# Optimization experiments

Measured on AMD Instinct MI355X. Metric: run time of the kernel, lower is better.

## Reference

```python
import jax, jax.numpy as jnp
import numpy as np

# Dimensions: B batches, E links, T time steps, F flows, rank-r factors, K unrolled iters
B, E, T, F = 16, 256, 4096, 512
RANK = 10
NUM_ITER = 5


def setup_inputs() -> dict:
    key = jax.random.key(0)
    ks = jax.random.split(key, 9)
    Y = jax.random.normal(ks[0], (B, E, T), dtype=jnp.float32)
    R = (jax.random.uniform(ks[1], (B, E, F)) < 0.1).astype(jnp.float32)
    Omega = (jax.random.uniform(ks[2], (B, E, T)) < 0.9).astype(jnp.float32)
    P0 = jax.random.normal(ks[3], (B, E, RANK), dtype=jnp.float32) * 0.1
    Q0 = jax.random.normal(ks[4], (B, T, RANK), dtype=jnp.float32) * 0.1
    # per-iteration learned log-parameters of the unrolled network
    lam_log = jax.random.normal(ks[5], (NUM_ITER,), dtype=jnp.float32) * 0.1 - 1.0
    mu_log = jax.random.normal(ks[6], (NUM_ITER,), dtype=jnp.float32) * 0.1 - 1.0
    nu_log = jax.random.normal(ks[7], (NUM_ITER,), dtype=jnp.float32) * 0.1
    gamma_logit = jax.random.normal(ks[8], (NUM_ITER,), dtype=jnp.float32) * 0.1
    return {"Y": Y, "R": R, "Omega": Omega, "P0": P0, "Q0": Q0,
            "lam_log": lam_log, "mu_log": mu_log, "nu_log": nu_log,
            "gamma_logit": gamma_logit}


def reference(Y, R, Omega, P0, Q0, lam_log, mu_log, nu_log, gamma_logit):
    """Unrolled BSCA: Y ~ X + R @ A + noise on observed entries (Omega mask),
    X relaxed low-rank via factors P (B,E,r), Q (B,T,r); A sparse anomalies (B,F,T).
    Each iteration: rank-r ridge solves for P and Q (left=False -> rhs @ inv(lhs)),
    relaxed X update, soft-thresholded BSCA direction for A + convex-combination step."""
    rank = P0.shape[-1]
    eye = jnp.eye(rank, dtype=Y.dtype)
    X = Omega * Y                     # (B,E,T) init relaxed variable
    A = jnp.zeros((*Y.shape[:-2], R.shape[-1], Y.shape[-1]), dtype=Y.dtype)  # (B,F,T)
    P, Q = P0, Q0
    A_scale = (R * R).mT @ (Omega * Omega)          # (B,F,T)
    noobs = A_scale == 0
    A_scale_safe = A_scale + noobs.astype(Y.dtype)
    for k in range(NUM_ITER):
        lam = jnp.exp(lam_log[k])
        mu = jnp.exp(mu_log[k])
        nu = jnp.exp(nu_log[k])
        gamma = jax.nn.sigmoid(gamma_logit[k])
        regp = lam / nu
        # P update: P = (X @ Q) @ inv(Q^T Q + regp I)   (right solve; lhs symmetric)
        lhsQ = Q.mT @ Q + regp * eye                 # (B,r,r)
        P = jnp.linalg.solve(lhsQ, (X @ Q).mT).mT    # (B,E,r)
        # Q update: Q = (X^T @ P) @ inv(P^T P + regp I)
        lhsP = P.mT @ P + regp * eye
        Q = jnp.linalg.solve(lhsP, (X.mT @ P).mT).mT # (B,T,r)
        # X update (relaxed): X = (Omega*err + nu*P Q^T) / (Omega^2 + nu)
        RA = R @ A                                   # (B,E,T)
        err = Omega * (Y - RA)
        X = (Omega * err + nu * (P @ Q.mT)) / (Omega * Omega + nu)
        # A update: soft-thresholded best-response + convex combination step
        resid = Omega * (Y - X - RA)                 # (B,E,T)
        BA = A + (R.mT @ resid) / A_scale_safe       # (B,F,T)
        A_dir = jnp.sign(BA) * jnp.maximum(jnp.abs(BA) - mu / A_scale_safe, 0.0)
        A_dir = jnp.where(noobs, 0.0, A_dir)
        A = A + gamma * (A_dir - A)
    return A
```

## Files before the change

### kernel.cpp

```cpp
#include <hip/hip_runtime.h>
#include <stdint.h>

#define BB 16
#define EE 256
#define TT 4096
#define FF 512
#define RK 10
#define NIT 5

typedef short bf16x8 __attribute__((ext_vector_type(8)));
typedef float f32x4  __attribute__((ext_vector_type(4)));

__device__ __forceinline__ unsigned short f2bf(float x){
  unsigned int u = __float_as_uint(x);
  unsigned int r = (u + 0x7FFFu + ((u >> 16) & 1u)) >> 16;
  return (unsigned short)r;
}
__device__ __forceinline__ float bf2f(unsigned short s){
  return __uint_as_float(((unsigned int)s) << 16);
}

__device__ __forceinline__ void gld16(const void* g, void* l){
  __builtin_amdgcn_global_load_lds((const __attribute__((address_space(1))) unsigned int*)g,
                                   (__attribute__((address_space(3))) unsigned int*)l,
                                   16, 0, 0);
}


__global__ void k_params(const float* lam_log, const float* mu_log,
                         const float* nu_log, const float* gl, float* prm){
  int k = threadIdx.x;
  if (k < NIT){
    float lam = expf(lam_log[k]);
    float mu  = expf(mu_log[k]);
    float nu  = expf(nu_log[k]);
    float gam = 1.0f/(1.0f+expf(-gl[k]));
    prm[k*8+0]=lam; prm[k*8+1]=mu; prm[k*8+2]=nu; prm[k*8+3]=gam; prm[k*8+4]=lam/nu;
  }
}

__global__ void k_initX(const float4* __restrict__ Y, const float4* __restrict__ Om,
                        float4* __restrict__ X, ushort4* __restrict__ Omb){
  int i = blockIdx.x*256 + threadIdx.x;
  float4 y = Y[i], o = Om[i];
  X[i] = make_float4(y.x*o.x, y.y*o.y, y.z*o.z, y.w*o.w);
  ushort4 ob; ob.x=f2bf(o.x); ob.y=f2bf(o.y); ob.z=f2bf(o.z); ob.w=f2bf(o.w);
  Omb[i] = ob;
}

__global__ void k_qtrans(const float* __restrict__ Q0, float* __restrict__ Qt){
  int idx = blockIdx.x*256 + threadIdx.x;
  int b = idx >> 12, t = idx & (TT-1);
  #pragma unroll
  for (int j=0;j<RK;j++)
    Qt[((size_t)b*RK + j)*TT + t] = Q0[(size_t)idx*RK + j];
}

__global__ void k_rbf(const float4* __restrict__ R, ushort4* __restrict__ Rb){
  int i = blockIdx.x*256 + threadIdx.x;
  float4 v = R[i];
  ushort4 o; o.x=f2bf(v.x); o.y=f2bf(v.y); o.z=f2bf(v.z); o.w=f2bf(v.w);
  Rb[i] = o;
}

__global__ void k_rtransb(const float* __restrict__ Rm, unsigned short* __restrict__ Rbt){
  int f = blockIdx.x, b = blockIdx.y, e = threadIdx.x;
  Rbt[((size_t)b*FF + f)*EE + e] = f2bf(Rm[((size_t)b*EE + e)*FF + f]);
}

__global__ void k_omtrans(const unsigned short* __restrict__ Omb,
                          unsigned short* __restrict__ OmbT){
  __shared__ unsigned short sT[64][66];
  int b  = blockIdx.z;
  int E0 = blockIdx.y*64, T0 = blockIdx.x*64;
  int tid = threadIdx.x;
  int fi = tid >> 4;
  int m  = tid & 15;
  #pragma unroll
  for (int pass=0; pass<4; ++pass){
    int e = pass*16 + fi;
    ushort4 v = *(const ushort4*)(Omb + ((size_t)(b*EE + E0 + e))*TT + T0 + m*4);
    sT[e][m*4+0]=v.x; sT[e][m*4+1]=v.y; sT[e][m*4+2]=v.z; sT[e][m*4+3]=v.w;
  }
  __syncthreads();
  #pragma unroll
  for (int pass=0; pass<4; ++pass){
    int t  = pass*16 + fi;
    int e4 = m*4;
    ushort4 o;
    o.x = sT[e4+0][t]; o.y = sT[e4+1][t];
    o.z = sT[e4+2][t]; o.w = sT[e4+3][t];
    *(ushort4*)(OmbT + ((size_t)b*TT + T0 + t)*EE + E0 + e4) = o;
  }
}


__global__ void k_lhsQ(const float* __restrict__ Qt, const float* __restrict__ prm,
                       float* __restrict__ lhs, int k){
  int p = blockIdx.x, b = blockIdx.y;
  int i = 0, rem = p;
  while (rem >= i+1){ rem -= (i+1); ++i; }
  int j = rem;
  const float* qi = Qt + ((size_t)b*RK + i)*TT;
  const float* qj = Qt + ((size_t)b*RK + j)*TT;
  float a = 0.0f;
  for (int t = threadIdx.x*4; t < TT; t += 1024){
    float4 x = *(const float4*)(qi+t);
    float4 y = *(const float4*)(qj+t);
    a += x.x*y.x + x.y*y.y + x.z*y.z + x.w*y.w;
  }
  __shared__ float red[256];
  red[threadIdx.x] = a; __syncthreads();
  for (int s=128; s>0; s>>=1){
    if (threadIdx.x < s) red[threadIdx.x] += red[threadIdx.x+s];
    __syncthreads();
  }
  if (threadIdx.x==0){
    float v = red[0];
    if (i==j) v += prm[k*8+4];
    lhs[(b*RK+i)*RK + j] = v;
    lhs[(b*RK+j)*RK + i] = v;
  }
}

__global__ void k_lhsP(const float* __restrict__ P, const float* __restrict__ prm,
                       float* __restrict__ lhs, int k){
  int p = blockIdx.x, b = blockIdx.y;
  int i = 0, rem = p;
  while (rem >= i+1){ rem -= (i+1); ++i; }
  int j = rem;
  int e = threadIdx.x;
  const float* pr = P + ((size_t)b*EE + e)*RK;
  float a = pr[i]*pr[j];
  __shared__ float red[256];
  red[threadIdx.x] = a; __syncthreads();
  for (int s=128; s>0; s>>=1){
    if (threadIdx.x < s) red[threadIdx.x] += red[threadIdx.x+s];
    __syncthreads();
  }
  if (threadIdx.x==0){
    float v = red[0];
    if (i==j) v += prm[k*8+4];
    lhs[(b*RK+i)*RK + j] = v;
    lhs[(b*RK+j)*RK + i] = v;
  }
}

__global__ void k_invert(const float* __restrict__ lhs, float* __restrict__ inv){
  int b = blockIdx.x;
  __shared__ float aug[RK][2*RK];
  int tid = threadIdx.x;
  int i = tid / (2*RK), j = tid % (2*RK);
  bool act = tid < RK*2*RK;
  if (act) aug[i][j] = (j < RK) ? lhs[(b*RK+i)*RK + j] : ((j-RK)==i ? 1.0f : 0.0f);
  __syncthreads();
  for (int kk=0; kk<RK; ++kk){
    float pinv = 1.0f / aug[kk][kk];
    __syncthreads();
    if (act && i==kk) aug[i][j] *= pinv;
    __syncthreads();
    float factor = (act && i!=kk) ? aug[i][kk] : 0.0f;
    float pivrow = act ? aug[kk][j] : 0.0f;
    __syncthreads();
    if (act && i!=kk) aug[i][j] -= factor * pivrow;
    __syncthreads();
  }
  if (act && j >= RK) inv[(b*RK+i)*RK + (j-RK)] = aug[i][j];
}

__global__ void k_Pupd(const float* __restrict__ X, const float* __restrict__ Qt,
                       const float* __restrict__ inv, float* __restrict__ P){
  int e = blockIdx.x, b = blockIdx.y;
  const float* xr = X + ((size_t)b*EE + e)*TT;
  const float* qb = Qt + (size_t)b*RK*TT;
  float acc[RK];
  #pragma unroll
  for (int j=0;j<RK;j++) acc[j]=0.0f;
  for (int t = threadIdx.x*4; t < TT; t += 1024){
    float4 x = *(const float4*)(xr+t);
    #pragma unroll
    for (int j=0;j<RK;j++){
      float4 q = *(const float4*)(qb + (size_t)j*TT + t);
      acc[j] += x.x*q.x + x.y*q.y + x.z*q.z + x.w*q.w;
    }
  }
  __shared__ float partial[4][RK];
  int lane = threadIdx.x & 63, wv = threadIdx.x >> 6;
  #pragma unroll
  for (int j=0;j<RK;j++){
    float v = acc[j];
    for (int s=32;s>0;s>>=1) v += __shfl_down(v, s, 64);
    if (lane==0) partial[wv][j] = v;
  }
  __syncthreads();
  if (threadIdx.x < RK){
    int i = threadIdx.x;
    float out = 0.0f;
    #pragma unroll
    for (int j=0;j<RK;j++){
      float xq = partial[0][j]+partial[1][j]+partial[2][j]+partial[3][j];
      out += xq * inv[(b*RK+j)*RK + i];
    }
    P[((size_t)b*EE + e)*RK + i] = out;
  }
}

__global__ void k_Qupd(const float* __restrict__ X, const float* __restrict__ P,
                       const float* __restrict__ inv, float* __restrict__ Qt){
  int b = blockIdx.y;
  int t = blockIdx.x*256 + threadIdx.x;
  __shared__ float sP[EE*RK];
  __shared__ float sInv[RK*RK];
  for (int i=threadIdx.x; i<EE*RK; i+=256) sP[i] = P[(size_t)b*EE*RK + i];
  if (threadIdx.x < RK*RK) sInv[threadIdx.x] = inv[b*RK*RK + threadIdx.x];
  __syncthreads();
  float acc[RK];
  #pragma unroll
  for (int j=0;j<RK;j++) acc[j]=0.0f;
  const float* xb = X + (size_t)b*EE*TT + t;
  for (int e=0;e<EE;e++){
    float x = xb[(size_t)e*TT];
    #pragma unroll
    for (int j=0;j<RK;j++) acc[j] += x * sP[e*RK+j];
  }
  #pragma unroll
  for (int i=0;i<RK;i++){
    float q = 0.0f;
    #pragma unroll
    for (int j=0;j<RK;j++) q += acc[j]*sInv[j*RK+i];
    Qt[((size_t)b*RK + i)*TT + t] = q;
  }
}

__global__ void k_atrans(const float* __restrict__ A, unsigned short* __restrict__ Abt){
  __shared__ float sT[64][65];
  int b  = blockIdx.z;
  int F0 = blockIdx.y*64, T0 = blockIdx.x*64;
  int tid = threadIdx.x;
  int fi = tid >> 4;
  int m  = tid & 15;
  #pragma unroll
  for (int pass=0; pass<4; ++pass){
    int f = pass*16 + fi;
    float4 v = *(const float4*)(A + ((size_t)(b*FF + F0 + f))*TT + T0 + m*4);
    sT[f][m*4+0]=v.x; sT[f][m*4+1]=v.y; sT[f][m*4+2]=v.z; sT[f][m*4+3]=v.w;
  }
  __syncthreads();
  #pragma unroll
  for (int pass=0; pass<4; ++pass){
    int t  = pass*16 + fi;
    int f4 = m*4;
    ushort4 o;
    o.x = f2bf(sT[f4+0][t]); o.y = f2bf(sT[f4+1][t]);
    o.z = f2bf(sT[f4+2][t]); o.w = f2bf(sT[f4+3][t]);
    *(ushort4*)(Abt + ((size_t)b*TT + T0 + t)*FF + F0 + f4) = o;
  }
}

__global__ __launch_bounds__(256) void k_gemm1m(
    const unsigned short* __restrict__ Rb, const unsigned short* __restrict__ Abt,
    const float* __restrict__ Y, const unsigned short* __restrict__ Omb,
    const float* __restrict__ Qt, const float* __restrict__ P,
    const float* __restrict__ prm, float* __restrict__ X,
    unsigned short* __restrict__ residT, int k)
{
  __shared__ __align__(16) unsigned char lds[20480];
  int id = blockIdx.x;
  int b  = id >> 6;
  int e0 = ((id >> 5) & 1) * 128;
  int t0 = (id & 31) * 128;
  int tid  = threadIdx.x;
  int lane = tid & 63, wid = tid >> 6;
  int lr = lane & 15, lg = lane >> 4;
  int wm = wid >> 1, wn = wid & 1;

  f32x4 acc[4][4];
  #pragma unroll
  for (int m=0;m<4;++m)
    #pragma unroll
    for (int n=0;n<4;++n)
      #pragma unroll
      for (int i=0;i<4;++i) acc[m][n][i]=0.0f;

  if (k > 0){
    int swz  = ((lg ^ (lr & 3)) << 4);
    int aoff = (wm*64 + lr)*64 + swz;
    int boff = 8192 + (wn*64 + lr)*64 + swz;
    int c0 = tid, c1 = tid + 256;
    int r0 = c0 >> 2, s0 = c0 & 3;
    int r1 = c1 >> 2, s1 = c1 & 3;
    const unsigned short* gA0 = Rb  + ((size_t)(b*EE + e0 + r0))*FF + ((s0 ^ (r0&3))<<3);
    const unsigned short* gA1 = Rb  + ((size_t)(b*EE + e0 + r1))*FF + ((s1 ^ (r1&3))<<3);
    const unsigned short* gB0 = Abt + ((size_t)b*TT + t0 + r0)*FF   + ((s0 ^ (r0&3))<<3);
    const unsigned short* gB1 = Abt + ((size_t)b*TT + t0 + r1)*FF   + ((s1 ^ (r1&3))<<3);
    unsigned char* lA0 = lds + c0*16;
    unsigned char* lA1 = lds + c1*16;
    unsigned char* lB0 = lds + 8192 + c0*16;
    unsigned char* lB1 = lds + 8192 + c1*16;

    for (int kk=0; kk<16; ++kk){
      __syncthreads();
      int f0 = kk*32;
      gld16(gA0 + f0, lA0);
      gld16(gA1 + f0, lA1);
      gld16(gB0 + f0, lB0);
      gld16(gB1 + f0, lB1);
      asm volatile("s_waitcnt vmcnt(0)" ::: "memory");
      __syncthreads();
      bf16x8 af[4], bb[4];
      #pragma unroll
      for (int m=0;m<4;++m) af[m] = *(const bf16x8*)(lds + aoff + m*1024);
      #pragma unroll
      for (int n=0;n<4;++n) bb[n] = *(const bf16x8*)(lds + boff + n*1024);
      #pragma unroll
      for (int m=0;m<4;++m)
        #pragma unroll
        for (int n=0;n<4;++n)
          acc[m][n] = __builtin_amdgcn_mfma_f32_16x16x32_bf16(af[m], bb[n], acc[m][n], 0, 0, 0);
    }
  }

  __syncthreads();
  unsigned short* wbuf = (unsigned short*)(lds + wid*2176);
  float* Pl = (float*)(lds + 8704);
  float* Ql = (float*)(lds + 8704 + 5120);
  for (int idx = tid; idx < 128*RK; idx += 256)
    Pl[idx] = P[((size_t)(b*EE + e0))*RK + idx];
  for (int idx = tid; idx < RK*128; idx += 256){
    int j = idx >> 7, t = idx & 127;
    Ql[idx] = Qt[((size_t)(b*RK + j))*TT + t0 + t];
  }
  __syncthreads();

  float nu = prm[k*8+2];
  #pragma unroll
  for (int n=0;n<4;++n){
    int tloc = wn*64 + n*16 + lr;
    float ql[RK];
    #pragma unroll
    for (int j=0;j<RK;++j) ql[j] = Ql[j*128 + tloc];
    asm volatile("" ::: "memory");
    #pragma unroll
    for (int m=0;m<4;++m){
      #pragma unroll
      for (int r=0;r<4;++r){
        int eloc = wm*64 + m*16 + lg*4 + r;
        float pq = 0.0f;
        #pragma unroll
        for (int j=0;j<RK;++j) pq += Pl[eloc*RK + j]*ql[j];
        float ra = acc[m][n][r];
        size_t off = ((size_t)(b*EE + e0 + eloc))*TT + t0 + tloc;
        float y = Y[off];
        float o = bf2f(Omb[off]);
        float d = y - ra, om2 = o*o;
        float x = (om2*d + nu*pq)/(om2 + nu);
        float rs = o*(y - x - ra);
        X[off] = x;
        wbuf[lr*68 + m*16 + lg*4 + r] = f2bf(rs);
      }
    }
    asm volatile("" ::: "memory");
    #pragma unroll
    for (int j2=0;j2<4;++j2){
      int row = j2*4 + lg;
      int c4  = lr*4;
      ushort4 vv = *(const ushort4*)(wbuf + row*68 + c4);
      *(ushort4*)(residT + ((size_t)b*TT + t0 + wn*64 + n*16 + row)*EE + e0 + wm*64 + c4) = vv;
    }
    asm volatile("" ::: "memory");
  }
}

__device__ __forceinline__ float aupd(float a, float g, unsigned short asu,
                                      float mu, float gamma){
  float as = bf2f(asu);
  bool no = (as == 0.0f);
  float rs = 1.0f / (no ? 1.0f : as);
  float ba = a + g*rs;
  float ad = copysignf(fmaxf(fabsf(ba) - mu*rs, 0.0f), ba);
  if (no) ad = 0.0f;
  return a + gamma*(ad - a);
}

__global__ __launch_bounds__(256) void k_gemm2m(
    const unsigned short* __restrict__ Rbt, const unsigned short* __restrict__ residT,
    const unsigned short* __restrict__ As, const float* __restrict__ prm,
    float* __restrict__ A, int k)
{
  __shared__ __align__(16) unsigned char lds[16384];
  int id = blockIdx.x;
  int b  = id >> 7;
  int f0 = ((id >> 5) & 3) * 128;
  int t0 = (id & 31) * 128;
  int tid  = threadIdx.x;
  int lane = tid & 63, wid = tid >> 6;
  int lr = lane & 15, lg = lane >> 4;
  int wm = wid >> 1, wn = wid & 1;

  f32x4 acc[4][4];
  #pragma unroll
  for (int m=0;m<4;++m)
    #pragma unroll
    for (int n=0;n<4;++n)
      #pragma unroll
      for (int i=0;i<4;++i) acc[m][n][i]=0.0f;

  int swz  = ((lg ^ (lr & 3)) << 4);
  int aoff = (wm*64 + lr)*64 + swz;
  int boff = 8192 + (wn*64 + lr)*64 + swz;
  int c0 = tid, c1 = tid + 256;
  int r0 = c0 >> 2, s0 = c0 & 3;
  int r1 = c1 >> 2, s1 = c1 & 3;
  const unsigned short* gA0 = Rbt    + ((size_t)(b*FF + f0 + r0))*EE + ((s0 ^ (r0&3))<<3);
  const unsigned short* gA1 = Rbt    + ((size_t)(b*FF + f0 + r1))*EE + ((s1 ^ (r1&3))<<3);
  const unsigned short* gB0 = residT + ((size_t)b*TT + t0 + r0)*EE   + ((s0 ^ (r0&3))<<3);
  const unsigned short* gB1 = residT + ((size_t)b*TT + t0 + r1)*EE   + ((s1 ^ (r1&3))<<3);
  unsigned char* lA0 = lds + c0*16;
  unsigned char* lA1 = lds + c1*16;
  unsigned char* lB0 = lds + 8192 + c0*16;
  unsigned char* lB1 = lds + 8192 + c1*16;

  for (int kk=0; kk<8; ++kk){
    __syncthreads();
    int eoff = kk*32;
    gld16(gA0 + eoff, lA0);
    gld16(gA1 + eoff, lA1);
    gld16(gB0 + eoff, lB0);
    gld16(gB1 + eoff, lB1);
    asm volatile("s_waitcnt vmcnt(0)" ::: "memory");
    __syncthreads();
    bf16x8 af[4], bb[4];
    #pragma unroll
    for (int m=0;m<4;++m) af[m] = *(const bf16x8*)(lds + aoff + m*1024);
    #pragma unroll
    for (int n=0;n<4;++n) bb[n] = *(const bf16x8*)(lds + boff + n*1024);
    #pragma unroll
    for (int m=0;m<4;++m)
      #pragma unroll
      for (int n=0;n<4;++n)
        acc[m][n] = __builtin_amdgcn_mfma_f32_16x16x32_bf16(af[m], bb[n], acc[m][n], 0, 0, 0);
  }

  float mu = prm[k*8+1], gamma = prm[k*8+3];
  #pragma unroll
  for (int m=0;m<4;++m){
    #pragma unroll
    for (int r=0;r<4;++r){
      int floc = wm*64 + m*16 + lg*4 + r;
      size_t rowoff = ((size_t)(b*FF + f0 + floc))*TT + t0;
      #pragma unroll
      for (int n=0;n<4;++n){
        int tloc = wn*64 + n*16 + lr;
        size_t off = rowoff + tloc;
        float a = A[off];
        A[off] = aupd(a, acc[m][n][r], As[off], mu, gamma);
      }
    }
  }
}

__global__ __launch_bounds__(256) void k_ascalem(
    const unsigned short* __restrict__ Rbt, const unsigned short* __restrict__ OmbT,
    unsigned short* __restrict__ As)
{
  __shared__ __align__(16) unsigned char lds[16384];
  int id = blockIdx.x;
  int b  = id >> 7;
  int f0 = ((id >> 5) & 3) * 128;
  int t0 = (id & 31) * 128;
  int tid  = threadIdx.x;
  int lane = tid & 63, wid = tid >> 6;
  int lr = lane & 15, lg = lane >> 4;
  int wm = wid >> 1, wn = wid & 1;

  f32x4 acc[4][4];
  #pragma unroll
  for (int m=0;m<4;++m)
    #pragma unroll
    for (int n=0;n<4;++n)
      #pragma unroll
      for (int i=0;i<4;++i) acc[m][n][i]=0.0f;

  int swz  = ((lg ^ (lr & 3)) << 4);
  int aoff = (wm*64 + lr)*64 + swz;
  int boff = 8192 + (wn*64 + lr)*64 + swz;
  int c0 = tid, c1 = tid + 256;
  int r0 = c0 >> 2, s0 = c0 & 3;
  int r1 = c1 >> 2, s1 = c1 & 3;
  const unsigned short* gA0 = Rbt  + ((size_t)(b*FF + f0 + r0))*EE + ((s0 ^ (r0&3))<<3);
  const unsigned short* gA1 = Rbt  + ((size_t)(b*FF + f0 + r1))*EE + ((s1 ^ (r1&3))<<3);
  const unsigned short* gB0 = OmbT + ((size_t)b*TT + t0 + r0)*EE   + ((s0 ^ (r0&3))<<3);
  const unsigned short* gB1 = OmbT + ((size_t)b*TT + t0 + r1)*EE   + ((s1 ^ (r1&3))<<3);
  unsigned char* lA0 = lds + c0*16;
  unsigned char* lA1 = lds + c1*16;
  unsigned char* lB0 = lds + 8192 + c0*16;
  unsigned char* lB1 = lds + 8192 + c1*16;

  for (int kk=0; kk<8; ++kk){
    __syncthreads();
    int eoff = kk*32;
    gld16(gA0 + eoff, lA0);
    gld16(gA1 + eoff, lA1);
    gld16(gB0 + eoff, lB0);
    gld16(gB1 + eoff, lB1);
    asm volatile("s_waitcnt vmcnt(0)" ::: "memory");
    __syncthreads();
    bf16x8 af[4], bb[4];
    #pragma unroll
    for (int m=0;m<4;++m) af[m] = *(const bf16x8*)(lds + aoff + m*1024);
    #pragma unroll
    for (int n=0;n<4;++n) bb[n] = *(const bf16x8*)(lds + boff + n*1024);
    #pragma unroll
    for (int m=0;m<4;++m)
      #pragma unroll
      for (int n=0;n<4;++n)
        acc[m][n] = __builtin_amdgcn_mfma_f32_16x16x32_bf16(af[m], bb[n], acc[m][n], 0, 0, 0);
  }

  #pragma unroll
  for (int m=0;m<4;++m){
    #pragma unroll
    for (int r=0;r<4;++r){
      int floc = wm*64 + m*16 + lg*4 + r;
      size_t rowoff = ((size_t)(b*FF + f0 + floc))*TT + t0;
      #pragma unroll
      for (int n=0;n<4;++n){
        int tloc = wn*64 + n*16 + lr;
        As[rowoff + tloc] = f2bf(acc[m][n][r]);
      }
    }
  }
}


extern "C" void kernel_launch(void* const* d_in, const int* in_sizes, int n_in,
                              void* d_out, int out_size, void* d_ws, size_t ws_size,
                              hipStream_t stream){
  const float* Y   = (const float*)d_in[0];
  const float* Rm  = (const float*)d_in[1];
  const float* Om  = (const float*)d_in[2];
  const float* P0  = (const float*)d_in[3];
  const float* Q0  = (const float*)d_in[4];
  const float* lam = (const float*)d_in[5];
  const float* mu  = (const float*)d_in[6];
  const float* nu  = (const float*)d_in[7];
  const float* gl  = (const float*)d_in[8];
  float* A = (float*)d_out;

  char* ws = (char*)d_ws;
  const size_t X_OFF    = 0;
  const size_t REST_OFF = X_OFF    + (size_t)BB*EE*TT*4;
  const size_t OMB_OFF  = REST_OFF + (size_t)BB*TT*EE*2;
  const size_t AS_OFF   = OMB_OFF  + (size_t)BB*EE*TT*2;
  const size_t QT_OFF   = AS_OFF   + (size_t)BB*FF*TT*2;
  const size_t P_OFF    = QT_OFF   + (size_t)BB*RK*TT*4;
  const size_t LHS_OFF  = P_OFF    + (size_t)BB*EE*RK*4;
  const size_t INV_OFF  = LHS_OFF  + (size_t)BB*RK*RK*4;
  const size_t PRM_OFF  = INV_OFF  + (size_t)BB*RK*RK*4;
  const size_t RB_OFF   = PRM_OFF  + 4096;
  const size_t RBT_OFF  = RB_OFF   + (size_t)BB*EE*FF*2;
  const size_t OMBT_OFF = RBT_OFF  + (size_t)BB*FF*EE*2;
  const size_t ABT_OFF  = OMBT_OFF + (size_t)BB*TT*EE*2;

  float* X    = (float*)(ws + X_OFF);
  unsigned short* residT = (unsigned short*)(ws + REST_OFF);
  unsigned short* Omb    = (unsigned short*)(ws + OMB_OFF);
  unsigned short* As     = (unsigned short*)(ws + AS_OFF);
  float* Qt   = (float*)(ws + QT_OFF);
  float* P    = (float*)(ws + P_OFF);
  float* lhs  = (float*)(ws + LHS_OFF);
  float* inv  = (float*)(ws + INV_OFF);
  float* prm  = (float*)(ws + PRM_OFF);
  unsigned short* Rb   = (unsigned short*)(ws + RB_OFF);
  unsigned short* Rbt  = (unsigned short*)(ws + RBT_OFF);
  unsigned short* OmbT = (unsigned short*)(ws + OMBT_OFF);
  unsigned short* Abt  = (unsigned short*)(ws + ABT_OFF);

  (void)P0; (void)Om; (void)in_sizes; (void)n_in; (void)ws_size;

  hipMemsetAsync(d_out, 0, (size_t)out_size*sizeof(float), stream);
  k_params<<<1, 64, 0, stream>>>(lam, mu, nu, gl, prm);
  k_initX<<<BB*EE*TT/4/256, 256, 0, stream>>>((const float4*)Y, (const float4*)Om,
                                              (float4*)X, (ushort4*)Omb);
  k_qtrans<<<BB*TT/256, 256, 0, stream>>>(Q0, Qt);
  k_rbf<<<BB*EE*FF/4/256, 256, 0, stream>>>((const float4*)Rm, (ushort4*)Rb);
  k_rtransb<<<dim3(FF, BB), 256, 0, stream>>>(Rm, Rbt);
  k_omtrans<<<dim3(TT/64, EE/64, BB), 256, 0, stream>>>(Omb, OmbT);
  k_ascalem<<<2048, 256, 0, stream>>>(Rbt, OmbT, As);

  for (int k=0; k<NIT; ++k){
    k_lhsQ  <<<dim3(55, BB), 256, 0, stream>>>(Qt, prm, lhs, k);
    k_invert<<<BB, 256, 0, stream>>>(lhs, inv);
    k_Pupd  <<<dim3(EE, BB), 256, 0, stream>>>(X, Qt, inv, P);
    k_lhsP  <<<dim3(55, BB), 256, 0, stream>>>(P, prm, lhs, k);
    k_invert<<<BB, 256, 0, stream>>>(lhs, inv);
    k_Qupd  <<<dim3(TT/256, BB), 256, 0, stream>>>(X, P, inv, Qt);
    if (k > 0)
      k_atrans<<<dim3(TT/64, FF/64, BB), 256, 0, stream>>>(A, Abt);
    k_gemm1m<<<BB*2*32, 256, 0, stream>>>(Rb, Abt, Y, Omb, Qt, P, prm, X, residT, k);
    k_gemm2m<<<2048, 256, 0, stream>>>(Rbt, residT, As, prm, A, k);
  }
}
```

Measured before the change: 1.993 ms.

## Fuse A transpose into gemm2 epilogue and swap MFMA operands for vectorized epilogues

Removes the separate k_atrans kernel: gemm2 now writes the bf16 transposed copy of A (Abt) straight from its epilogue through an LDS staging buffer, skipping it on the last iteration. The MFMA operand order is swapped in all three GEMMs so each lane owns four consecutive t values, which lets the epilogues use float4/ushort4 global loads and stores instead of scalar ones. The LDS swizzle gains an extra XOR term to cut bank conflicts. The cost is extra LDS traffic and another barrier in the gemm2 epilogue.

New measurement: 1.797 ms. 1.11x faster.

```diff
diff --git a/kernel.cpp b/kernel.cpp
--- a/kernel.cpp
+++ b/kernel.cpp
@@ -24,6 +24,10 @@
   __builtin_amdgcn_global_load_lds((const __attribute__((address_space(1))) unsigned int*)g,
                                    (__attribute__((address_space(3))) unsigned int*)l,
                                    16, 0, 0);
+}
+
+__device__ __forceinline__ int ssw(int r, int s){
+  return ((s ^ (r & 3) ^ ((r >> 2) & 3)) << 3);
 }
 
 
@@ -232,33 +236,8 @@
   }
 }
 
-__global__ void k_atrans(const float* __restrict__ A, unsigned short* __restrict__ Abt){
-  __shared__ float sT[64][65];
-  int b  = blockIdx.z;
-  int F0 = blockIdx.y*64, T0 = blockIdx.x*64;
-  int tid = threadIdx.x;
-  int fi = tid >> 4;
-  int m  = tid & 15;
-  #pragma unroll
-  for (int pass=0; pass<4; ++pass){
-    int f = pass*16 + fi;
-    float4 v = *(const float4*)(A + ((size_t)(b*FF + F0 + f))*TT + T0 + m*4);
-    sT[f][m*4+0]=v.x; sT[f][m*4+1]=v.y; sT[f][m*4+2]=v.z; sT[f][m*4+3]=v.w;
-  }
-  __syncthreads();
-  #pragma unroll
-  for (int pass=0; pass<4; ++pass){
-    int t  = pass*16 + fi;
-    int f4 = m*4;
-    ushort4 o;
-    o.x = f2bf(sT[f4+0][t]); o.y = f2bf(sT[f4+1][t]);
-    o.z = f2bf(sT[f4+2][t]); o.w = f2bf(sT[f4+3][t]);
-    *(ushort4*)(Abt + ((size_t)b*TT + T0 + t)*FF + F0 + f4) = o;
-  }
-}
-
 __global__ __launch_bounds__(256) void k_gemm1m(
-    const unsigned short* __restrict__ Rb, const unsigned short* __restrict__ Abt,
+    const unsigned short* __restrict__ Abt, const unsigned short* __restrict__ Rb,
     const float* __restrict__ Y, const unsigned short* __restrict__ Omb,
     const float* __restrict__ Qt, const float* __restrict__ P,
     const float* __restrict__ prm, float* __restrict__ X,
@@ -283,16 +262,16 @@
       for (int i=0;i<4;++i) acc[m][n][i]=0.0f;
 
   if (k > 0){
-    int swz  = ((lg ^ (lr & 3)) << 4);
+    int swz  = ((lg ^ (lr & 3) ^ ((lr >> 2) & 3)) << 4);
     int aoff = (wm*64 + lr)*64 + swz;
     int boff = 8192 + (wn*64 + lr)*64 + swz;
     int c0 = tid, c1 = tid + 256;
     int r0 = c0 >> 2, s0 = c0 & 3;
     int r1 = c1 >> 2, s1 = c1 & 3;
-    const unsigned short* gA0 = Rb  + ((size_t)(b*EE + e0 + r0))*FF + ((s0 ^ (r0&3))<<3);
-    const unsigned short* gA1 = Rb  + ((size_t)(b*EE + e0 + r1))*FF + ((s1 ^ (r1&3))<<3);
-    const unsigned short* gB0 = Abt + ((size_t)b*TT + t0 + r0)*FF   + ((s0 ^ (r0&3))<<3);
-    const unsigned short* gB1 = Abt + ((size_t)b*TT + t0 + r1)*FF   + ((s1 ^ (r1&3))<<3);
+    const unsigned short* gA0 = Abt + ((size_t)b*TT + t0 + r0)*FF + ssw(r0,s0);
+    const unsigned short* gA1 = Abt + ((size_t)b*TT + t0 + r1)*FF + ssw(r1,s1);
+    const unsigned short* gB0 = Rb  + ((size_t)(b*EE + e0 + r0))*FF + ssw(r0,s0);
+    const unsigned short* gB1 = Rb  + ((size_t)(b*EE + e0 + r1))*FF + ssw(r1,s1);
     unsigned char* lA0 = lds + c0*16;
     unsigned char* lA1 = lds + c1*16;
     unsigned char* lB0 = lds + 8192 + c0*16;
@@ -300,11 +279,11 @@
 
     for (int kk=0; kk<16; ++kk){
       __syncthreads();
-      int f0 = kk*32;
-      gld16(gA0 + f0, lA0);
-      gld16(gA1 + f0, lA1);
-      gld16(gB0 + f0, lB0);
-      gld16(gB1 + f0, lB1);
+      int f0k = kk*32;
+      gld16(gA0 + f0k, lA0);
+      gld16(gA1 + f0k, lA1);
+      gld16(gB0 + f0k, lB0);
+      gld16(gB1 + f0k, lB1);
       asm volatile("s_waitcnt vmcnt(0)" ::: "memory");
       __syncthreads();
       bf16x8 af[4], bb[4];
@@ -334,30 +313,47 @@
 
   float nu = prm[k*8+2];
   #pragma unroll
-  for (int n=0;n<4;++n){
-    int tloc = wn*64 + n*16 + lr;
-    float ql[RK];
-    #pragma unroll
-    for (int j=0;j<RK;++j) ql[j] = Ql[j*128 + tloc];
+  for (int m=0;m<4;++m){
+    int tq = wm*64 + m*16 + lg*4;
+    float4 ql4[RK];
+    #pragma unroll
+    for (int j=0;j<RK;++j) ql4[j] = *(const float4*)(Ql + j*128 + tq);
     asm volatile("" ::: "memory");
     #pragma unroll
-    for (int m=0;m<4;++m){
-      #pragma unroll
-      for (int r=0;r<4;++r){
-        int eloc = wm*64 + m*16 + lg*4 + r;
-        float pq = 0.0f;
-        #pragma unroll
-        for (int j=0;j<RK;++j) pq += Pl[eloc*RK + j]*ql[j];
-        float ra = acc[m][n][r];
-        size_t off = ((size_t)(b*EE + e0 + eloc))*TT + t0 + tloc;
-        float y = Y[off];
-        float o = bf2f(Omb[off]);
-        float d = y - ra, om2 = o*o;
-        float x = (om2*d + nu*pq)/(om2 + nu);
-        float rs = o*(y - x - ra);
-        X[off] = x;
-        wbuf[lr*68 + m*16 + lg*4 + r] = f2bf(rs);
+    for (int n=0;n<4;++n){
+      int eloc = wn*64 + n*16 + lr;
+      const float* pr = Pl + eloc*RK;
+      float4 pq = {0,0,0,0};
+      #pragma unroll
+      for (int j=0;j<RK;++j){
+        float pj = pr[j];
+        pq.x += pj*ql4[j].x; pq.y += pj*ql4[j].y;
+        pq.z += pj*ql4[j].z; pq.w += pj*ql4[j].w;
       }
+      f32x4 ra = acc[m][n];
+      size_t off = ((size_t)(b*EE + e0 + eloc))*TT + t0 + tq;
+      float4 y = *(const float4*)(Y + off);
+      ushort4 ou = *(const ushort4*)(Omb + off);
+      float4 xo; float rs0, rs1, rs2, rs3;
+      {
+        float o = bf2f(ou.x), om2 = o*o, d = y.x - ra[0];
+        xo.x = (om2*d + nu*pq.x)/(om2 + nu); rs0 = o*(y.x - xo.x - ra[0]);
+      }{
+        float o = bf2f(ou.y), om2 = o*o, d = y.y - ra[1];
+        xo.y = (om2*d + nu*pq.y)/(om2 + nu); rs1 = o*(y.y - xo.y - ra[1]);
+      }{
+        float o = bf2f(ou.z), om2 = o*o, d = y.z - ra[2];
+        xo.z = (om2*d + nu*pq.z)/(om2 + nu); rs2 = o*(y.z - xo.z - ra[2]);
+      }{
+        float o = bf2f(ou.w), om2 = o*o, d = y.w - ra[3];
+        xo.w = (om2*d + nu*pq.w)/(om2 + nu); rs3 = o*(y.w - xo.w - ra[3]);
+      }
+      *(float4*)(X + off) = xo;
+      int wc = n*16 + lr;
+      wbuf[(lg*4+0)*68 + wc] = f2bf(rs0);
+      wbuf[(lg*4+1)*68 + wc] = f2bf(rs1);
+      wbuf[(lg*4+2)*68 + wc] = f2bf(rs2);
+      wbuf[(lg*4+3)*68 + wc] = f2bf(rs3);
     }
     asm volatile("" ::: "memory");
     #pragma unroll
@@ -365,7 +361,7 @@
       int row = j2*4 + lg;
       int c4  = lr*4;
       ushort4 vv = *(const ushort4*)(wbuf + row*68 + c4);
-      *(ushort4*)(residT + ((size_t)b*TT + t0 + wn*64 + n*16 + row)*EE + e0 + wm*64 + c4) = vv;
+      *(ushort4*)(residT + ((size_t)b*TT + t0 + wm*64 + m*16 + row)*EE + e0 + wn*64 + c4) = vv;
     }
     asm volatile("" ::: "memory");
   }
@@ -383,9 +379,9 @@
 }
 
 __global__ __launch_bounds__(256) void k_gemm2m(
-    const unsigned short* __restrict__ Rbt, const unsigned short* __restrict__ residT,
+    const unsigned short* __restrict__ residT, const unsigned short* __restrict__ Rbt,
     const unsigned short* __restrict__ As, const float* __restrict__ prm,
-    float* __restrict__ A, int k)
+    float* __restrict__ A, unsigned short* __restrict__ Abt, int k)
 {
   __shared__ __align__(16) unsigned char lds[16384];
   int id = blockIdx.x;
@@ -405,16 +401,16 @@
       #pragma unroll
       for (int i=0;i<4;++i) acc[m][n][i]=0.0f;
 
-  int swz  = ((lg ^ (lr & 3)) << 4);
+  int swz  = ((lg ^ (lr & 3) ^ ((lr >> 2) & 3)) << 4);
   int aoff = (wm*64 + lr)*64 + swz;
   int boff = 8192 + (wn*64 + lr)*64 + swz;
   int c0 = tid, c1 = tid + 256;
   int r0 = c0 >> 2, s0 = c0 & 3;
   int r1 = c1 >> 2, s1 = c1 & 3;
-  const unsigned short* gA0 = Rbt    + ((size_t)(b*FF + f0 + r0))*EE + ((s0 ^ (r0&3))<<3);
-  const unsigned short* gA1 = Rbt    + ((size_t)(b*FF + f0 + r1))*EE + ((s1 ^ (r1&3))<<3);
-  const unsigned short* gB0 = residT + ((size_t)b*TT + t0 + r0)*EE   + ((s0 ^ (r0&3))<<3);
-  const unsigned short* gB1 = residT + ((size_t)b*TT + t0 + r1)*EE   + ((s1 ^ (r1&3))<<3);
+  const unsigned short* gA0 = residT + ((size_t)b*TT + t0 + r0)*EE + ssw(r0,s0);
+  const unsigned short* gA1 = residT + ((size_t)b*TT + t0 + r1)*EE + ssw(r1,s1);
+  const unsigned short* gB0 = Rbt    + ((size_t)(b*FF + f0 + r0))*EE + ssw(r0,s0);
+  const unsigned short* gB1 = Rbt    + ((size_t)(b*FF + f0 + r1))*EE + ssw(r1,s1);
   unsigned char* lA0 = lds + c0*16;
   unsigned char* lA1 = lds + c1*16;
   unsigned char* lB0 = lds + 8192 + c0*16;
@@ -441,26 +437,50 @@
         acc[m][n] = __builtin_amdgcn_mfma_f32_16x16x32_bf16(af[m], bb[n], acc[m][n], 0, 0, 0);
   }
 
+  __syncthreads();
+  unsigned short* wbuf = (unsigned short*)(lds + wid*2176);
   float mu = prm[k*8+1], gamma = prm[k*8+3];
+  bool emit = (k < NIT-1);
   #pragma unroll
   for (int m=0;m<4;++m){
-    #pragma unroll
-    for (int r=0;r<4;++r){
-      int floc = wm*64 + m*16 + lg*4 + r;
-      size_t rowoff = ((size_t)(b*FF + f0 + floc))*TT + t0;
-      #pragma unroll
-      for (int n=0;n<4;++n){
-        int tloc = wn*64 + n*16 + lr;
-        size_t off = rowoff + tloc;
-        float a = A[off];
-        A[off] = aupd(a, acc[m][n][r], As[off], mu, gamma);
+    int tq = wm*64 + m*16 + lg*4;
+    #pragma unroll
+    for (int n=0;n<4;++n){
+      int floc = wn*64 + n*16 + lr;
+      size_t off = ((size_t)(b*FF + f0 + floc))*TT + t0 + tq;
+      float4 a = *(const float4*)(A + off);
+      ushort4 as4 = *(const ushort4*)(As + off);
+      f32x4 g = acc[m][n];
+      float4 an;
+      an.x = aupd(a.x, g[0], as4.x, mu, gamma);
+      an.y = aupd(a.y, g[1], as4.y, mu, gamma);
+      an.z = aupd(a.z, g[2], as4.z, mu, gamma);
+      an.w = aupd(a.w, g[3], as4.w, mu, gamma);
+      *(float4*)(A + off) = an;
+      if (emit){
+        int wc = n*16 + lr;
+        wbuf[(lg*4+0)*68 + wc] = f2bf(an.x);
+        wbuf[(lg*4+1)*68 + wc] = f2bf(an.y);
+        wbuf[(lg*4+2)*68 + wc] = f2bf(an.z);
+        wbuf[(lg*4+3)*68 + wc] = f2bf(an.w);
       }
     }
+    asm volatile("" ::: "memory");
+    if (emit){
+      #pragma unroll
+      for (int j2=0;j2<4;++j2){
+        int row = j2*4 + lg;
+        int c4  = lr*4;
+        ushort4 vv = *(const ushort4*)(wbuf + row*68 + c4);
+        *(ushort4*)(Abt + ((size_t)b*TT + t0 + wm*64 + m*16 + row)*FF + f0 + wn*64 + c4) = vv;
+      }
+    }
+    asm volatile("" ::: "memory");
   }
 }
 
 __global__ __launch_bounds__(256) void k_ascalem(
-    const unsigned short* __restrict__ Rbt, const unsigned short* __restrict__ OmbT,
+    const unsigned short* __restrict__ OmbT, const unsigned short* __restrict__ Rbt,
     unsigned short* __restrict__ As)
 {
   __shared__ __align__(16) unsigned char lds[16384];
@@ -481,16 +501,16 @@
       #pragma unroll
       for (int i=0;i<4;++i) acc[m][n][i]=0.0f;
 
-  int swz  = ((lg ^ (lr & 3)) << 4);
+  int swz  = ((lg ^ (lr & 3) ^ ((lr >> 2) & 3)) << 4);
   int aoff = (wm*64 + lr)*64 + swz;
   int boff = 8192 + (wn*64 + lr)*64 + swz;
   int c0 = tid, c1 = tid + 256;
   int r0 = c0 >> 2, s0 = c0 & 3;
   int r1 = c1 >> 2, s1 = c1 & 3;
-  const unsigned short* gA0 = Rbt  + ((size_t)(b*FF + f0 + r0))*EE + ((s0 ^ (r0&3))<<3);
-  const unsigned short* gA1 = Rbt  + ((size_t)(b*FF + f0 + r1))*EE + ((s1 ^ (r1&3))<<3);
-  const unsigned short* gB0 = OmbT + ((size_t)b*TT + t0 + r0)*EE   + ((s0 ^ (r0&3))<<3);
-  const unsigned short* gB1 = OmbT + ((size_t)b*TT + t0 + r1)*EE   + ((s1 ^ (r1&3))<<3);
+  const unsigned short* gA0 = OmbT + ((size_t)b*TT + t0 + r0)*EE + ssw(r0,s0);
+  const unsigned short* gA1 = OmbT + ((size_t)b*TT + t0 + r1)*EE + ssw(r1,s1);
+  const unsigned short* gB0 = Rbt  + ((size_t)(b*FF + f0 + r0))*EE + ssw(r0,s0);
+  const unsigned short* gB1 = Rbt  + ((size_t)(b*FF + f0 + r1))*EE + ssw(r1,s1);
   unsigned char* lA0 = lds + c0*16;
   unsigned char* lA1 = lds + c1*16;
   unsigned char* lB0 = lds + 8192 + c0*16;
@@ -519,15 +539,15 @@
 
   #pragma unroll
   for (int m=0;m<4;++m){
-    #pragma unroll
-    for (int r=0;r<4;++r){
-      int floc = wm*64 + m*16 + lg*4 + r;
-      size_t rowoff = ((size_t)(b*FF + f0 + floc))*TT + t0;
-      #pragma unroll
-      for (int n=0;n<4;++n){
-        int tloc = wn*64 + n*16 + lr;
-        As[rowoff + tloc] = f2bf(acc[m][n][r]);
-      }
+    int tq = wm*64 + m*16 + lg*4;
+    #pragma unroll
+    for (int n=0;n<4;++n){
+      int floc = wn*64 + n*16 + lr;
+      size_t off = ((size_t)(b*FF + f0 + floc))*TT + t0 + tq;
+      ushort4 o;
+      o.x = f2bf(acc[m][n][0]); o.y = f2bf(acc[m][n][1]);
+      o.z = f2bf(acc[m][n][2]); o.w = f2bf(acc[m][n][3]);
+      *(ushort4*)(As + off) = o;
     }
   }
 }
@@ -586,7 +606,7 @@
   k_rbf<<<BB*EE*FF/4/256, 256, 0, stream>>>((const float4*)Rm, (ushort4*)Rb);
   k_rtransb<<<dim3(FF, BB), 256, 0, stream>>>(Rm, Rbt);
   k_omtrans<<<dim3(TT/64, EE/64, BB), 256, 0, stream>>>(Omb, OmbT);
-  k_ascalem<<<2048, 256, 0, stream>>>(Rbt, OmbT, As);
+  k_ascalem<<<2048, 256, 0, stream>>>(OmbT, Rbt, As);
 
   for (int k=0; k<NIT; ++k){
     k_lhsQ  <<<dim3(55, BB), 256, 0, stream>>>(Qt, prm, lhs, k);
@@ -595,9 +615,7 @@
     k_lhsP  <<<dim3(55, BB), 256, 0, stream>>>(P, prm, lhs, k);
     k_invert<<<BB, 256, 0, stream>>>(lhs, inv);
     k_Qupd  <<<dim3(TT/256, BB), 256, 0, stream>>>(X, P, inv, Qt);
-    if (k > 0)
-      k_atrans<<<dim3(TT/64, FF/64, BB), 256, 0, stream>>>(A, Abt);
-    k_gemm1m<<<BB*2*32, 256, 0, stream>>>(Rb, Abt, Y, Omb, Qt, P, prm, X, residT, k);
-    k_gemm2m<<<2048, 256, 0, stream>>>(Rbt, residT, As, prm, A, k);
-  }
-}
+    k_gemm1m<<<BB*2*32, 256, 0, stream>>>(Abt, Rb, Y, Omb, Qt, P, prm, X, residT, k);
+    k_gemm2m<<<2048, 256, 0, stream>>>(residT, Rbt, As, prm, A, Abt, k);
+  }
+}
```
